# Kernel optimization log

Measured on AMD Instinct MI355X. Metric: run time of the kernel, lower is better.

The kernel has to match this reference:

```python
import jax, jax.numpy as jnp
import numpy as np

KSIZE = 7   # pooled output grid (kernel_size)
SR = 2      # bilinear sampling ratio per bin side


def setup_inputs() -> dict:
    key = jax.random.key(0)
    k1, k2, k3 = jax.random.split(key, 3)
    B, H, W, C = 8, 64, 64, 256
    N = 4096
    x = jax.random.normal(k1, (B, H, W, C), jnp.float32)
    # random valid boxes in feature-map coordinates: (y1, x1, y2, x2), y2 > y1
    raw = jax.random.uniform(k2, (N, 4), jnp.float32)
    c1 = raw[:, :2] * jnp.array([H - 1.0, W - 1.0], jnp.float32)
    c2 = raw[:, 2:] * jnp.array([H - 1.0, W - 1.0], jnp.float32)
    lo = jnp.minimum(c1, c2)
    hi = jnp.maximum(c1, c2) + 1.0  # ensure non-degenerate boxes
    rois = jnp.stack([lo[:, 0], lo[:, 1], hi[:, 0], hi[:, 1]], axis=1)
    batch_idx = jax.random.randint(k3, (N,), 0, B, jnp.int32)
    return {"x": x, "rois": rois, "batch_idx": batch_idx}


def reference(x, rois, batch_idx):
    """ROIAlign: per-ROI bilinear sampling + average pooling.

    x:         [B, H, W, C] feature map (channels-last)
    rois:      [N, 4] boxes (y1, x1, y2, x2) in feature-map pixel coords
    batch_idx: [N] int index of the image each ROI belongs to
    returns:   [N, KSIZE, KSIZE, C]
    """
    B, H, W, C = x.shape
    N = rois.shape[0]
    K, S = KSIZE, KSIZE * SR  # S x S sample points per ROI

    y1, x1, y2, x2 = rois[:, 0], rois[:, 1], rois[:, 2], rois[:, 3]
    bin_h = (y2 - y1) / K
    bin_w = (x2 - x1) / K

    # sample coordinate s within ROI: y1 + (s + 0.5)/SR * bin_h, s in [0, S)
    off = (jnp.arange(S, dtype=x.dtype) + 0.5) / SR          # [S]
    sy = y1[:, None] + off[None, :] * bin_h[:, None]          # [N, S]
    sx = x1[:, None] + off[None, :] * bin_w[:, None]          # [N, S]

    yy = sy[:, :, None]                                       # [N, S, 1]
    xx = sx[:, None, :]                                       # [N, 1, S]
    y0 = jnp.clip(jnp.floor(yy), 0, H - 2).astype(jnp.int32)  # [N, S, 1]
    x0 = jnp.clip(jnp.floor(xx), 0, W - 2).astype(jnp.int32)  # [N, 1, S]
    ly = jnp.clip(yy - y0, 0.0, 1.0)                          # [N, S, 1]
    lx = jnp.clip(xx - x0, 0.0, 1.0)                          # [N, 1, S]

    b = batch_idx[:, None, None]                              # [N, 1, 1]
    # gather 4 bilinear corners -> each [N, S, S, C]
    v00 = x[b, y0, x0]
    v01 = x[b, y0, x0 + 1]
    v10 = x[b, y0 + 1, x0]
    v11 = x[b, y0 + 1, x0 + 1]

    ly_ = ly[..., None]  # [N, S, 1, 1]
    lx_ = lx[..., None]  # [N, 1, S, 1]
    val = (v00 * (1 - ly_) * (1 - lx_) + v01 * (1 - ly_) * lx_
           + v10 * ly_ * (1 - lx_) + v11 * ly_ * lx_)          # [N, S, S, C]

    # average-pool the SR x SR samples inside each of the K x K bins
    out = val.reshape(N, K, SR, K, SR, C).mean(axis=(2, 4))   # [N, K, K, C]
    return out
```

## Files before the change

### kernel.cpp

```cpp
#include <hip/hip_runtime.h>

#define KSIZE 7
#define NBINS (KSIZE * KSIZE)
#define NMAX  4096
#define BMAX  8

typedef float v4f __attribute__((ext_vector_type(4)));

constexpr int C4c  = 64;
constexpr int WC4c = 4096;

__global__ __launch_bounds__(256) void bucket_kernel(
    const int* __restrict__ bi, int* __restrict__ assign, int N, int B, int cap)
{
    __shared__ int cnt[BMAX];
    __shared__ int ovf_n, ovf_c;
    __shared__ int asg[NMAX];
    __shared__ int ovf[NMAX];

    const int t = threadIdx.x;
    if (t < BMAX) cnt[t] = 0;
    if (t == 0) { ovf_n = 0; ovf_c = 0; }
    for (int i = t; i < N; i += 256) asg[i] = -1;
    __syncthreads();

    for (int i = t; i < N; i += 256) {
        int k = bi[i];
        int p = atomicAdd(&cnt[k], 1);
        if (p < cap) asg[p * B + k] = i;
        else { int q = atomicAdd(&ovf_n, 1); ovf[q] = i; }
    }
    __syncthreads();

    for (int i = t; i < N; i += 256) {
        if (asg[i] < 0) { int q = atomicAdd(&ovf_c, 1); asg[i] = ovf[q]; }
    }
    __syncthreads();

    for (int i = t; i < N; i += 256) assign[i] = asg[i];
}

__global__ __launch_bounds__(256, 3) void roialign_kernel(
    const float* __restrict__ x,
    const float* __restrict__ rois,
    const int*   __restrict__ batch_idx,
    float*       __restrict__ out,
    const int*   __restrict__ assign,
    int H, int W, int C)
{
    __shared__ int   ridx[4][KSIZE][4];
    __shared__ float rwgt[4][KSIZE][4];
    __shared__ int   cidx[4][KSIZE][4];
    __shared__ float cwgt[4][KSIZE][4];
    __shared__ int   rn[4][KSIZE];
    __shared__ int   cn[4][KSIZE];

    const int t    = threadIdx.x;
    const int lane = t & 63;
    const int wave = t >> 6;

    const int n = assign[blockIdx.x];
    const float4 rb = ((const float4*)rois)[n];
    const int bimg  = batch_idx[n];

    const float bin_h = (rb.z - rb.x) / (float)KSIZE;
    const float bin_w = (rb.w - rb.y) / (float)KSIZE;

    {
        const bool isrow = (lane < KSIZE);
        const bool iscol = (lane >= 16) && (lane < 16 + KSIZE);
        if (isrow || iscol) {
            const int   k    = isrow ? lane : lane - 16;
            const float base = isrow ? rb.x : rb.y;
            const float bsz  = isrow ? bin_h : bin_w;
            const int   dim  = isrow ? H : W;

            const float sA = base + ((float)k + 0.25f) * bsz;
            const float sB = base + ((float)k + 0.75f) * bsz;
            const float fA = fminf(fmaxf(floorf(sA), 0.0f), (float)(dim - 2));
            const float fB = fminf(fmaxf(floorf(sB), 0.0f), (float)(dim - 2));
            const int   iA = (int)fA,  iB = (int)fB;
            const float lA = fminf(fmaxf(sA - fA, 0.0f), 1.0f);
            const float lB = fminf(fmaxf(sB - fB, 0.0f), 1.0f);

            int   i0 = iA,     i1 = iA + 1, i2, i3, cnt_;
            float w0 = (1.0f - lA) * 0.5f, w1 = lA * 0.5f, w2, w3;
            if (iB == iA) {
                w0 += (1.0f - lB) * 0.5f;
                w1 += lB * 0.5f;
                i2 = iA; w2 = 0.0f;
                i3 = iA; w3 = 0.0f;
                cnt_ = 2;
            } else if (iB == iA + 1) {
                w1 += (1.0f - lB) * 0.5f;
                i2 = iB + 1; w2 = lB * 0.5f;
                i3 = iA;     w3 = 0.0f;
                cnt_ = 3;
            } else {
                i2 = iB;     w2 = (1.0f - lB) * 0.5f;
                i3 = iB + 1; w3 = lB * 0.5f;
                cnt_ = 4;
            }
            if (isrow) {
                ridx[wave][k][0] = i0; ridx[wave][k][1] = i1;
                ridx[wave][k][2] = i2; ridx[wave][k][3] = i3;
                rwgt[wave][k][0] = w0; rwgt[wave][k][1] = w1;
                rwgt[wave][k][2] = w2; rwgt[wave][k][3] = w3;
                rn[wave][k] = cnt_;
            } else {
                cidx[wave][k][0] = i0; cidx[wave][k][1] = i1;
                cidx[wave][k][2] = i2; cidx[wave][k][3] = i3;
                cwgt[wave][k][0] = w0; cwgt[wave][k][1] = w1;
                cwgt[wave][k][2] = w2; cwgt[wave][k][3] = w3;
                cn[wave][k] = cnt_;
            }
        }
    }
    asm volatile("s_waitcnt lgkmcnt(0)" ::: "memory");

    const v4f* __restrict__ xbase =
        (const v4f*)x + (size_t)bimg * 64 * WC4c + lane;
    float* __restrict__ outn = out + (size_t)n * (NBINS * 256);

    v4f vA[16], vB[16];
    #pragma unroll
    for (int i = 0; i < 16; ++i) {
        vA[i] = (v4f){0.f, 0.f, 0.f, 0.f};
        vB[i] = (v4f){0.f, 0.f, 0.f, 0.f};
    }

#define LR2(RV, RP) V[(RV)*4+0] = (RP)[c0_]; V[(RV)*4+1] = (RP)[c1_];
#define LR3(RV, RP) LR2(RV, RP) V[(RV)*4+2] = (RP)[c2_];
#define LR4(RV, RP) LR3(RV, RP) V[(RV)*4+3] = (RP)[c3_];
#define LDN2(NC) LR##NC(0, r0_) LR##NC(1, r1_)
#define LDN3(NC) LDN2(NC) LR##NC(2, r2_)
#define LDN4(NC) LDN3(NC) LR##NC(3, r3_)

#define ISSUE(VARR, KY, KX)                                                 \
    do {                                                                    \
        v4f (&V)[16] = VARR;                                                \
        const v4f* r0_ = xbase + ridx[wave][KY][0] * WC4c;                  \
        const v4f* r1_ = xbase + ridx[wave][KY][1] * WC4c;                  \
        const v4f* r2_ = xbase + ridx[wave][KY][2] * WC4c;                  \
        const v4f* r3_ = xbase + ridx[wave][KY][3] * WC4c;                  \
        const int c0_ = cidx[wave][KX][0] * C4c;                            \
        const int c1_ = cidx[wave][KX][1] * C4c;                            \
        const int c2_ = cidx[wave][KX][2] * C4c;                            \
        const int c3_ = cidx[wave][KX][3] * C4c;                            \
        const int code_ = (rn[wave][KY] - 2) * 3 + (cn[wave][KX] - 2);      \
        switch (code_) {                                                    \
        case 0: { LDN2(2) } break;                                          \
        case 1: { LDN2(3) } break;                                          \
        case 2: { LDN2(4) } break;                                          \
        case 3: { LDN3(2) } break;                                          \
        case 4: { LDN3(3) } break;                                          \
        case 5: { LDN3(4) } break;                                          \
        case 6: { LDN4(2) } break;                                          \
        case 7: { LDN4(3) } break;                                          \
        default: { LDN4(4) } break;                                         \
        }                                                                   \
    } while (0)

#define COMPUTE(VARR, BIN, KY, KX)                                          \
    do {                                                                    \
        v4f (&V)[16] = VARR;                                                \
        v4f acc = {0.f, 0.f, 0.f, 0.f};                                     \
        _Pragma("unroll")                                                   \
        for (int r_ = 0; r_ < 4; ++r_) {                                    \
            const float wr_ = rwgt[wave][KY][r_];                           \
            acc += V[r_*4+0] * (wr_ * cwgt[wave][KX][0]);                   \
            acc += V[r_*4+1] * (wr_ * cwgt[wave][KX][1]);                   \
            acc += V[r_*4+2] * (wr_ * cwgt[wave][KX][2]);                   \
            acc += V[r_*4+3] * (wr_ * cwgt[wave][KX][3]);                   \
        }                                                                   \
        v4f* op_ = (v4f*)(outn + (size_t)(BIN) * 256) + lane;               \
        __builtin_nontemporal_store(acc, op_);                              \
    } while (0)

    int bin = wave;
    int kyA = bin / KSIZE, kxA = bin - kyA * KSIZE;
    int kyB, kxB;
    ISSUE(vA, kyA, kxA);
    for (;;) {
        int nb = bin + 4;
        if (nb < NBINS) {
            kyB = nb / KSIZE; kxB = nb - kyB * KSIZE;
            ISSUE(vB, kyB, kxB);
            COMPUTE(vA, bin, kyA, kxA);
            bin = nb;
        } else {
            COMPUTE(vA, bin, kyA, kxA);
            break;
        }
        nb = bin + 4;
        if (nb < NBINS) {
            kyA = nb / KSIZE; kxA = nb - kyA * KSIZE;
            ISSUE(vA, kyA, kxA);
            COMPUTE(vB, bin, kyB, kxB);
            bin = nb;
        } else {
            COMPUTE(vB, bin, kyB, kxB);
            break;
        }
    }
#undef ISSUE
#undef COMPUTE
#undef LR2
#undef LR3
#undef LR4
#undef LDN2
#undef LDN3
#undef LDN4
}

extern "C" void kernel_launch(void* const* d_in, const int* in_sizes, int n_in,
                              void* d_out, int out_size, void* d_ws, size_t ws_size,
                              hipStream_t stream) {
    const float* x         = (const float*)d_in[0];
    const float* rois      = (const float*)d_in[1];
    const int*   batch_idx = (const int*)d_in[2];
    float*       out       = (float*)d_out;
    int*         assign    = (int*)d_ws;

    const int H = 64, W = 64, C = 256;
    const int N = in_sizes[1] / 4;
    const int B = in_sizes[0] / (H * W * C);
    const int cap = N / B;

    bucket_kernel<<<1, 256, 0, stream>>>(batch_idx, assign, N, B, cap);
    roialign_kernel<<<N, 256, 0, stream>>>(x, rois, batch_idx, out, assign,
                                           H, W, C);
}
```

Before: 297.4 us.

## Drop register double-buffering in favor of higher occupancy per CU

Replaces the software-pipelined A/B register buffers, which prefetched the next bin's 16 corner vectors while computing the current one, with a simple loop that loads and accumulates each bin directly. The launch bound minimum blocks per CU goes from 3 to 8, so the compiler must cap register use and more waves can be resident. The intent is to hide gather latency through wave-level parallelism instead of explicit prefetch. The cost is that each wave now stalls on its own loads with no overlap inside the wave.

Measured after the change: 384.0 us. +29.1%, slower.

```diff
diff --git a/kernel.cpp b/kernel.cpp
--- a/kernel.cpp
+++ b/kernel.cpp
@@ -40,7 +40,7 @@
     for (int i = t; i < N; i += 256) assign[i] = asg[i];
 }
 
-__global__ __launch_bounds__(256, 3) void roialign_kernel(
+__global__ __launch_bounds__(256, 8) void roialign_kernel(
     const float* __restrict__ x,
     const float* __restrict__ rois,
     const int*   __restrict__ batch_idx,
@@ -122,95 +122,63 @@
         (const v4f*)x + (size_t)bimg * 64 * WC4c + lane;
     float* __restrict__ outn = out + (size_t)n * (NBINS * 256);
 
-    v4f vA[16], vB[16];
-    #pragma unroll
-    for (int i = 0; i < 16; ++i) {
-        vA[i] = (v4f){0.f, 0.f, 0.f, 0.f};
-        vB[i] = (v4f){0.f, 0.f, 0.f, 0.f};
-    }
-
-#define LR2(RV, RP) V[(RV)*4+0] = (RP)[c0_]; V[(RV)*4+1] = (RP)[c1_];
-#define LR3(RV, RP) LR2(RV, RP) V[(RV)*4+2] = (RP)[c2_];
-#define LR4(RV, RP) LR3(RV, RP) V[(RV)*4+3] = (RP)[c3_];
-#define LDN2(NC) LR##NC(0, r0_) LR##NC(1, r1_)
-#define LDN3(NC) LDN2(NC) LR##NC(2, r2_)
-#define LDN4(NC) LDN3(NC) LR##NC(3, r3_)
-
-#define ISSUE(VARR, KY, KX)                                                 \
-    do {                                                                    \
-        v4f (&V)[16] = VARR;                                                \
-        const v4f* r0_ = xbase + ridx[wave][KY][0] * WC4c;                  \
-        const v4f* r1_ = xbase + ridx[wave][KY][1] * WC4c;                  \
-        const v4f* r2_ = xbase + ridx[wave][KY][2] * WC4c;                  \
-        const v4f* r3_ = xbase + ridx[wave][KY][3] * WC4c;                  \
-        const int c0_ = cidx[wave][KX][0] * C4c;                            \
-        const int c1_ = cidx[wave][KX][1] * C4c;                            \
-        const int c2_ = cidx[wave][KX][2] * C4c;                            \
-        const int c3_ = cidx[wave][KX][3] * C4c;                            \
-        const int code_ = (rn[wave][KY] - 2) * 3 + (cn[wave][KX] - 2);      \
-        switch (code_) {                                                    \
-        case 0: { LDN2(2) } break;                                          \
-        case 1: { LDN2(3) } break;                                          \
-        case 2: { LDN2(4) } break;                                          \
-        case 3: { LDN3(2) } break;                                          \
-        case 4: { LDN3(3) } break;                                          \
-        case 5: { LDN3(4) } break;                                          \
-        case 6: { LDN4(2) } break;                                          \
-        case 7: { LDN4(3) } break;                                          \
-        default: { LDN4(4) } break;                                         \
-        }                                                                   \
-    } while (0)
-
-#define COMPUTE(VARR, BIN, KY, KX)                                          \
-    do {                                                                    \
-        v4f (&V)[16] = VARR;                                                \
-        v4f acc = {0.f, 0.f, 0.f, 0.f};                                     \
-        _Pragma("unroll")                                                   \
-        for (int r_ = 0; r_ < 4; ++r_) {                                    \
-            const float wr_ = rwgt[wave][KY][r_];                           \
-            acc += V[r_*4+0] * (wr_ * cwgt[wave][KX][0]);                   \
-            acc += V[r_*4+1] * (wr_ * cwgt[wave][KX][1]);                   \
-            acc += V[r_*4+2] * (wr_ * cwgt[wave][KX][2]);                   \
-            acc += V[r_*4+3] * (wr_ * cwgt[wave][KX][3]);                   \
-        }                                                                   \
-        v4f* op_ = (v4f*)(outn + (size_t)(BIN) * 256) + lane;               \
-        __builtin_nontemporal_store(acc, op_);                              \
-    } while (0)
+#define ROW2(RV, RP)                                                        \
+    do { const float wr_ = rwgt[wave][ky][RV];                              \
+         v4f a_ = (RP)[c0_], b_ = (RP)[c1_];                                \
+         acc += a_ * (wr_ * cw0_) + b_ * (wr_ * cw1_); } while (0)
+#define ROW3(RV, RP)                                                        \
+    do { const float wr_ = rwgt[wave][ky][RV];                              \
+         v4f a_ = (RP)[c0_], b_ = (RP)[c1_], c_ = (RP)[c2_];                \
+         acc += a_ * (wr_ * cw0_) + b_ * (wr_ * cw1_)                       \
+              + c_ * (wr_ * cw2_); } while (0)
+#define ROW4(RV, RP)                                                        \
+    do { const float wr_ = rwgt[wave][ky][RV];                              \
+         v4f a_ = (RP)[c0_], b_ = (RP)[c1_], c_ = (RP)[c2_],                \
+             d_ = (RP)[c3_];                                                \
+         acc += a_ * (wr_ * cw0_) + b_ * (wr_ * cw1_)                       \
+              + c_ * (wr_ * cw2_) + d_ * (wr_ * cw3_); } while (0)
 
     int bin = wave;
-    int kyA = bin / KSIZE, kxA = bin - kyA * KSIZE;
-    int kyB, kxB;
-    ISSUE(vA, kyA, kxA);
+    int ky = 0, kx = wave;
     for (;;) {
-        int nb = bin + 4;
-        if (nb < NBINS) {
-            kyB = nb / KSIZE; kxB = nb - kyB * KSIZE;
-            ISSUE(vB, kyB, kxB);
-            COMPUTE(vA, bin, kyA, kxA);
-            bin = nb;
-        } else {
-            COMPUTE(vA, bin, kyA, kxA);
-            break;
+        const v4f* r0_ = xbase + ridx[wave][ky][0] * WC4c;
+        const v4f* r1_ = xbase + ridx[wave][ky][1] * WC4c;
+        const v4f* r2_ = xbase + ridx[wave][ky][2] * WC4c;
+        const v4f* r3_ = xbase + ridx[wave][ky][3] * WC4c;
+        const int c0_ = cidx[wave][kx][0] * C4c;
+        const int c1_ = cidx[wave][kx][1] * C4c;
+        const int c2_ = cidx[wave][kx][2] * C4c;
+        const int c3_ = cidx[wave][kx][3] * C4c;
+        const float cw0_ = cwgt[wave][kx][0];
+        const float cw1_ = cwgt[wave][kx][1];
+        const float cw2_ = cwgt[wave][kx][2];
+        const float cw3_ = cwgt[wave][kx][3];
+
+        v4f acc = {0.f, 0.f, 0.f, 0.f};
+        const int code_ = (rn[wave][ky] - 2) * 3 + (cn[wave][kx] - 2);
+        switch (code_) {
+        case 0: ROW2(0, r0_); ROW2(1, r1_); break;
+        case 1: ROW3(0, r0_); ROW3(1, r1_); break;
+        case 2: ROW4(0, r0_); ROW4(1, r1_); break;
+        case 3: ROW2(0, r0_); ROW2(1, r1_); ROW2(2, r2_); break;
+        case 4: ROW3(0, r0_); ROW3(1, r1_); ROW3(2, r2_); break;
+        case 5: ROW4(0, r0_); ROW4(1, r1_); ROW4(2, r2_); break;
+        case 6: ROW2(0, r0_); ROW2(1, r1_); ROW2(2, r2_); ROW2(3, r3_); break;
+        case 7: ROW3(0, r0_); ROW3(1, r1_); ROW3(2, r2_); ROW3(3, r3_); break;
+        default: ROW4(0, r0_); ROW4(1, r1_); ROW4(2, r2_); ROW4(3, r3_); break;
         }
-        nb = bin + 4;
-        if (nb < NBINS) {
-            kyA = nb / KSIZE; kxA = nb - kyA * KSIZE;
-            ISSUE(vA, kyA, kxA);
-            COMPUTE(vB, bin, kyB, kxB);
-            bin = nb;
-        } else {
-            COMPUTE(vB, bin, kyB, kxB);
-            break;
-        }
-    }
-#undef ISSUE
-#undef COMPUTE
-#undef LR2
-#undef LR3
-#undef LR4
-#undef LDN2
-#undef LDN3
-#undef LDN4
+
+        v4f* op_ = (v4f*)(outn + (size_t)bin * 256) + lane;
+        __builtin_nontemporal_store(acc, op_);
+
+        bin += 4;
+        if (bin >= NBINS) break;
+        kx += 4;
+        if (kx >= KSIZE) { kx -= KSIZE; ++ky; }
+    }
+#undef ROW2
+#undef ROW3
+#undef ROW4
 }
 
 extern "C" void kernel_launch(void* const* d_in, const int* in_sizes, int n_in,
```
